# Kernel optimization log

Hardware: AMD Instinct MI355X
Metric: run time of the kernel (lower is better)

Reference implementation:

```python
import jax, jax.numpy as jnp
import numpy as np

EPS = 1e-5
NUM_HEADS = 8


def _ln(x, g, b):
    m = x.mean(-1, keepdims=True)
    v = jnp.mean((x - m) ** 2, -1, keepdims=True)
    return (x - m) * jax.lax.rsqrt(v + EPS) * g + b


def _bn(x, g, b, m, v):  # eval-mode BatchNorm2d on NCHW
    sh = (1, -1, 1, 1)
    return (x - m.reshape(sh)) * jax.lax.rsqrt(v.reshape(sh) + EPS) * g.reshape(sh) + b.reshape(sh)


def _conv3x3(x, w):
    return jax.lax.conv_general_dilated(x, w, (1, 1), 'SAME', dimension_numbers=('NCHW', 'OIHW', 'NCHW'))


def _gelu(x):
    return jax.nn.gelu(x, approximate=False)  # torch nn.GELU default (erf)


def _attention(x, w_qkv, temperature, w_proj):
    # XCiT-style cross-covariance (channel) attention
    B, N, C = x.shape
    h = NUM_HEADS
    d = C // h
    qkv = (x @ w_qkv.T).reshape(B, N, 3, h, d)
    qkv = jnp.transpose(qkv, (2, 0, 3, 4, 1))  # [3, B, h, d, N]
    q, k, v = qkv[0], qkv[1], qkv[2]
    q = q / jnp.maximum(jnp.linalg.norm(q, axis=-1, keepdims=True), 1e-12)
    k = k / jnp.maximum(jnp.linalg.norm(k, axis=-1, keepdims=True), 1e-12)
    attn = jnp.einsum('bhdn,bhen->bhde', q, k) * temperature[None, :, None, None]
    attn = jax.nn.softmax(attn, axis=-1)  # [B, h, d, d]
    out = jnp.einsum('bhde,bhen->bhdn', attn, v)
    out = jnp.transpose(out, (0, 3, 1, 2)).reshape(B, N, C)
    return out @ w_proj.T


def _forward(x, ln1_g, ln1_b, w_qkv, temperature, w_proj, gamma1,
             ln2_g, ln2_b, mlp_w1, bn1_g, bn1_b, bn1_m, bn1_v,
             mlp_w2, bn2_g, bn2_b, bn2_m, bn2_v, gamma2,
             ln3_g, ln3_b, pconv1, pbn_g, pbn_b, pbn_m, pbn_v, pconv2, gamma3,
             H, W):
    B, N, C = x.shape
    # --- Attention residual block ---
    z = _attention(_ln(x, ln1_g, ln1_b), w_qkv, temperature, w_proj)
    x = x + gamma1 * z
    # --- ConvMlp residual block (1x1 convs + eval BN) ---
    y = _ln(x, ln2_g, ln2_b)
    y = jnp.transpose(y, (0, 2, 1)).reshape(B, C, H, W)
    y = _bn(jnp.einsum('oc,bchw->bohw', mlp_w1, y), bn1_g, bn1_b, bn1_m, bn1_v)
    y = _gelu(y)
    y = _bn(jnp.einsum('oc,bchw->bohw', mlp_w2, y), bn2_g, bn2_b, bn2_m, bn2_v)
    y = jnp.transpose(y.reshape(B, C, N), (0, 2, 1))
    x = x + gamma2 * y
    # --- Projection residual block (3x3 conv + BN + GELU + 3x3 conv) ---
    p = _ln(x, ln3_g, ln3_b)
    p = jnp.transpose(p, (0, 2, 1)).reshape(B, C, H, W)
    p = _conv3x3(p, pconv1)
    p = _gelu(_bn(p, pbn_g, pbn_b, pbn_m, pbn_v))
    p = _conv3x3(p, pconv2)
    p = jnp.transpose(p.reshape(B, C, N), (0, 2, 1))
    x = x + gamma3 * p
    return x


def setup_inputs() -> dict:
    key = jax.random.key(0)
    B, H, W, C, MR = 16, 48, 48, 384, 2
    N = H * W
    C2 = C * MR
    ks = jax.random.split(key, 12)
    nrm = lambda k, sh, s: (jax.random.normal(k, sh) * s).astype(jnp.float32)
    INIT_VALUES = 1e-4  # ResidualBlock default gamma init
    return {
        'x': nrm(ks[0], (B, N, C), 1.0),
        'ln1_g': jnp.ones((C,), jnp.float32), 'ln1_b': jnp.zeros((C,), jnp.float32),
        'w_qkv': nrm(ks[1], (3 * C, C), C ** -0.5),
        'temperature': jnp.ones((NUM_HEADS,), jnp.float32),
        'w_proj': nrm(ks[2], (C, C), C ** -0.5),
        'gamma1': jnp.full((C,), INIT_VALUES, jnp.float32),
        'ln2_g': jnp.ones((C,), jnp.float32), 'ln2_b': jnp.zeros((C,), jnp.float32),
        'mlp_w1': nrm(ks[3], (C2, C), C ** -0.5),
        'bn1_g': jnp.ones((C2,), jnp.float32), 'bn1_b': jnp.zeros((C2,), jnp.float32),
        'bn1_m': nrm(ks[4], (C2,), 0.1), 'bn1_v': jnp.ones((C2,), jnp.float32),
        'mlp_w2': nrm(ks[5], (C, C2), C2 ** -0.5),
        'bn2_g': jnp.ones((C,), jnp.float32), 'bn2_b': jnp.zeros((C,), jnp.float32),
        'bn2_m': nrm(ks[6], (C,), 0.1), 'bn2_v': jnp.ones((C,), jnp.float32),
        'gamma2': jnp.full((C,), INIT_VALUES, jnp.float32),
        'ln3_g': jnp.ones((C,), jnp.float32), 'ln3_b': jnp.zeros((C,), jnp.float32),
        'pconv1': nrm(ks[7], (C, C, 3, 3), (9 * C) ** -0.5),
        'pbn_g': jnp.ones((C,), jnp.float32), 'pbn_b': jnp.zeros((C,), jnp.float32),
        'pbn_m': nrm(ks[8], (C,), 0.1), 'pbn_v': jnp.ones((C,), jnp.float32),
        'pconv2': nrm(ks[9], (C, C, 3, 3), (9 * C) ** -0.5),
        'gamma3': jnp.full((C,), INIT_VALUES, jnp.float32),
        'H': H, 'W': W,
    }


def reference(x, ln1_g, ln1_b, w_qkv, temperature, w_proj, gamma1,
              ln2_g, ln2_b, mlp_w1, bn1_g, bn1_b, bn1_m, bn1_v,
              mlp_w2, bn2_g, bn2_b, bn2_m, bn2_v, gamma2,
              ln3_g, ln3_b, pconv1, pbn_g, pbn_b, pbn_m, pbn_v, pconv2, gamma3,
              H, W):
    out = _forward(x, ln1_g, ln1_b, w_qkv, temperature, w_proj, gamma1,
                   ln2_g, ln2_b, mlp_w1, bn1_g, bn1_b, bn1_m, bn1_v,
                   mlp_w2, bn2_g, bn2_b, bn2_m, bn2_v, gamma2,
                   ln3_g, ln3_b, pconv1, pbn_g, pbn_b, pbn_m, pbn_v, pconv2, gamma3,
                   H, W)
    return (out, H, W)
```

## Files before the change

kernel.cpp:

```cpp
#include <hip/hip_runtime.h>
#include <hip/hip_bf16.h>

typedef unsigned short u16;
typedef unsigned char  u8;
typedef __attribute__((ext_vector_type(4))) float floatx4;

#define LN_EPS 1e-5f

__device__ __forceinline__ float bf2f(u16 u) {
    unsigned int i = ((unsigned int)u) << 16;
    float f; __builtin_memcpy(&f, &i, 4); return f;
}
__device__ __forceinline__ u16 f2bf(float f) {
    __hip_bfloat16 h = __float2bfloat16(f);
    u16 u; __builtin_memcpy(&u, &h, 2); return u;
}
__device__ __forceinline__ u8 f2e4(float f) {
    int p = __builtin_amdgcn_cvt_pk_fp8_f32(f, f, 0, false);
    return (u8)(p & 0xff);
}

__device__ __forceinline__ int swz(int m, int k) {
    return (k & ~63) | (((((k >> 3) + (m >> 1)) & 7) << 3)) | (k & 7);
}

__device__ __forceinline__ void gl_lds16(const u8* g, u8* l) {
    __builtin_amdgcn_global_load_lds(
        (const __attribute__((address_space(1))) void*)(const void*)g,
        (__attribute__((address_space(3))) void*)(void*)l,
        16, 0, 0);
}

__global__ void cvt_f2e4_kernel(const float* __restrict__ in, u8* __restrict__ out,
                                int n4, int Kp) {
    int i = blockIdx.x * blockDim.x + threadIdx.x;
    if (i < n4) {
        float4 f = ((const float4*)in)[i];
        uchar4 o; o.x = f2e4(f.x); o.y = f2e4(f.y); o.z = f2e4(f.z); o.w = f2e4(f.w);
        int e = i * 4;
        int n = e / Kp, k = e - n * Kp;
        *(uchar4*)(out + (size_t)n * Kp + swz(n, k)) = o;
    }
}

__global__ void zero_kernel(u16* __restrict__ p, int n) {
    int i = blockIdx.x * blockDim.x + threadIdx.x;
    if (i < n) p[i] = 0;
}

__global__ void zero_f32_kernel(float* __restrict__ p, int n) {
    int i = blockIdx.x * blockDim.x + threadIdx.x;
    if (i < n) p[i] = 0.f;
}

template<bool SWZ>
__global__ __launch_bounds__(64)
void ln_kernel(const float* __restrict__ xf, const float* __restrict__ g,
               const float* __restrict__ b, u8* __restrict__ out) {
    const int row = blockIdx.x;
    const int lane = threadIdx.x;
    const float* xr = xf + (size_t)row * 384;
    float v[6], s = 0.f, s2 = 0.f;
#pragma unroll
    for (int i = 0; i < 6; ++i) { v[i] = xr[lane + i * 64]; s += v[i]; s2 += v[i] * v[i]; }
#pragma unroll
    for (int off = 32; off; off >>= 1) { s += __shfl_xor(s, off); s2 += __shfl_xor(s2, off); }
    float mean = s * (1.0f / 384.0f);
    float var  = s2 * (1.0f / 384.0f) - mean * mean;
    float rstd = rsqrtf(var + LN_EPS);
    u8* orow = out + (size_t)row * 384;
    int pofs = lane;
    if (SWZ) {
        const int gperm = (row >> 1) & 7;
        pofs = ((((lane >> 3) + gperm) & 7) << 3) | (lane & 7);
    }
#pragma unroll
    for (int i = 0; i < 6; ++i) {
        int c = lane + i * 64;
        orow[i * 64 + pofs] = f2e4((v[i] - mean) * rstd * g[c] + b[c]);
    }
}

template<int ACONV, int EPI, bool SWZO = false>
__global__ __launch_bounds__(256, 4)
void gemm_nt(const u8* __restrict__ A, const u8* __restrict__ Bm,
             int M, int N, int K,
             u16* __restrict__ Obf, int ldo,
             float* __restrict__ xf, float* __restrict__ ofb, const float* __restrict__ xin,
             const float* __restrict__ bn_g, const float* __restrict__ bn_b,
             const float* __restrict__ bn_m, const float* __restrict__ bn_v,
             const float* __restrict__ gamma, const u8* __restrict__ zp) {
    __shared__ u8 As[2][128 * 64];
    __shared__ u8 Bs[2][128 * 64];

    const int tid = threadIdx.x;
    const int gx = gridDim.x;
    const int g  = blockIdx.y * gx + blockIdx.x;
    const int G  = gx * gridDim.y;
    int L = g;
    if ((G & 7) == 0) L = (g & 7) * (G >> 3) + (g >> 3);
    const int n0 = (L % gx) * 128;
    const int m0 = (L / gx) * 128;

    const int lane  = tid & 63;
    const int wave  = tid >> 6;
    const int wm    = (wave >> 1) * 64;
    const int wn    = (wave & 1) * 64;
    const int fr    = lane & 15;
    const int klane = lane >> 4;

    int arow[4], brow[4];
#pragma unroll
    for (int i = 0; i < 4; ++i) {
        arow[i] = (wm + i * 16 + fr) * 64;
        brow[i] = (wn + i * 16 + fr) * 64;
    }
    int csw8[2];
#pragma unroll
    for (int kh = 0; kh < 2; ++kh)
        csw8[kh] = ((((kh << 2) + klane) + (fr >> 1)) & 7) << 3;
    int csw4[2];
#pragma unroll
    for (int kh = 0; kh < 2; ++kh)
        csw4[kh] = ((((kh << 1) + (klane >> 1) + (fr >> 1)) & 3) << 4) + ((klane & 1) << 3);

    const int srow = tid >> 2;
    const int scol = (tid & 3) << 4;
    const int ssc4 = ((((tid & 3) - ((tid >> 3) & 3)) & 3) << 4);
    const u8 *sa[2], *sb[2];
    const u8* imgq[2];
    int ay[2], ax[2];
#pragma unroll
    for (int q = 0; q < 2; ++q) {
        int r = q * 64 + srow;
        if (ACONV == 0) {
            sa[q] = A + (size_t)(m0 + r) * K + scol;
        } else {
            int nA = m0 + r;
            int bi = nA / 2304;
            int nl = nA - bi * 2304;
            ay[q] = nl / 48;
            ax[q] = nl - ay[q] * 48;
            imgq[q] = A + (size_t)bi * 2304 * 384;
        }
        sb[q] = Bm + (size_t)(n0 + q * 64 + srow) * K + scol;
    }

    int scnt = 0, sjj = 0;
    const int NT = K / 64;

    auto STAGE = [&](int d) {
        if (ACONV == 1) {
            if (scnt == 0) {
                int t3 = sjj / 3;
                int dy = t3 - 1, dx = sjj - t3 * 3 - 1;
                ++sjj;
#pragma unroll
                for (int q = 0; q < 2; ++q) {
                    int yy = ay[q] + dy, xx = ax[q] + dx;
                    bool v = ((unsigned)yy < 48u) & ((unsigned)xx < 48u);
                    sa[q] = (v ? imgq[q] + (size_t)(yy * 48 + xx) * 384 : zp) + ssc4;
                }
            }
            scnt = (scnt == 5) ? 0 : scnt + 1;
        }
        u8* la = &As[d][0];
        u8* lb = &Bs[d][0];
        gl_lds16(sa[0], la + ((wave * 64) << 4));        sa[0] += 64;
        gl_lds16(sa[1], la + ((256 + wave * 64) << 4));  sa[1] += 64;
        gl_lds16(sb[0], lb + ((wave * 64) << 4));        sb[0] += 64;
        gl_lds16(sb[1], lb + ((256 + wave * 64) << 4));  sb[1] += 64;
    };

    floatx4 acc[4][4];
#pragma unroll
    for (int i = 0; i < 4; ++i)
#pragma unroll
        for (int j = 0; j < 4; ++j) acc[i][j] = (floatx4){0.f, 0.f, 0.f, 0.f};

    STAGE(0);
    STAGE(1);
    asm volatile("s_waitcnt vmcnt(4)" ::: "memory");
    __builtin_amdgcn_s_barrier();
    asm volatile("" ::: "memory");

    int cur = 0;
    for (int t = 0; t < NT; ++t) {
        const u8* Ab = &As[cur][0];
        const u8* Bb = &Bs[cur][0];
#pragma unroll
        for (int kh = 0; kh < 2; ++kh) {
            long af[4], bfr[4];
#pragma unroll
            for (int i = 0; i < 4; ++i) af[i]  = *(const long*)(Ab + arow[i] + (ACONV ? csw4[kh] : csw8[kh]));
#pragma unroll
            for (int j = 0; j < 4; ++j)  bfr[j] = *(const long*)(Bb + brow[j] + csw8[kh]);
#pragma unroll
            for (int i = 0; i < 4; ++i)
#pragma unroll
                for (int j = 0; j < 4; ++j)
                    acc[i][j] = __builtin_amdgcn_mfma_f32_16x16x32_fp8_fp8(af[i], bfr[j], acc[i][j], 0, 0, 0);
        }
        asm volatile("s_waitcnt lgkmcnt(0)" ::: "memory");
        __builtin_amdgcn_s_barrier();
        asm volatile("" ::: "memory");
        if (t + 2 < NT) {
            STAGE(cur);
            asm volatile("s_waitcnt vmcnt(4)" ::: "memory");
        } else {
            asm volatile("s_waitcnt vmcnt(0)" ::: "memory");
        }
        __builtin_amdgcn_sched_barrier(0);
        __builtin_amdgcn_s_barrier();
        asm volatile("" ::: "memory");
        cur ^= 1;
    }

    const int quad4 = (lane >> 4) * 4;
#pragma unroll
    for (int j = 0; j < 4; ++j) {
        int col = n0 + wn + j * 16 + fr;
        float bscale = 0.f, bshift = 0.f, gam = 0.f;
        if (EPI == 1 || EPI == 2) {
            bscale = bn_g[col] * rsqrtf(bn_v[col] + LN_EPS);
            bshift = bn_b[col] - bn_m[col] * bscale;
        }
        if (EPI >= 2) gam = gamma[col];
#pragma unroll
        for (int i = 0; i < 4; ++i) {
#pragma unroll
            for (int r = 0; r < 4; ++r) {
                int row = m0 + wm + i * 16 + quad4 + r;
                float v = acc[i][j][r];
                if (EPI == 0) {
                    Obf[(size_t)row * ldo + col] = f2bf(v);
                } else if (EPI == 1) {
                    float t = v * bscale + bshift;
                    t = 0.5f * t * (1.0f + erff(t * 0.70710678118654752f));
                    int oc = SWZO ? swz(row, col) : col;
                    ((u8*)Obf)[(size_t)row * ldo + oc] = f2e4(t);
                } else if (EPI == 2) {
                    float t = v * bscale + bshift;
                    xf[(size_t)row * N + col] += gam * t;
                } else if (EPI == 3) {
                    xf[(size_t)row * N + col] += gam * v;
                } else if (EPI == 4) {
                    ofb[(size_t)row * N + col] = xf[(size_t)row * N + col] + gam * v;
                } else {
                    xf[(size_t)row * N + col] = xin[(size_t)row * N + col] + gam * v;
                }
            }
        }
    }
}

__global__ __launch_bounds__(256)
void gram_kernel(const u16* __restrict__ qkv, float* __restrict__ Sacc,
                 float* __restrict__ nrm2) {
    const int bh = blockIdx.y;
    const int b = bh >> 3, h = bh & 7;
    const int tid = threadIdx.x;
    __shared__ float qsf[64][48];
    __shared__ float ksf[64][48];

    float acc9[3][3];
#pragma unroll
    for (int i = 0; i < 3; ++i)
#pragma unroll
        for (int j = 0; j < 3; ++j) acc9[i][j] = 0.f;
    float qn2 = 0.f, kn2 = 0.f;

    const int qoff = h * 48;
    const int koff = 384 + h * 48;
    const int d0 = (tid >> 4) * 3;
    const int e0 = (tid & 15) * 3;
    const int nbase = blockIdx.x * 128;

    for (int c = 0; c < 2; ++c) {
        const int n0 = nbase + c * 64;
#pragma unroll
        for (int it = 0; it < 6; ++it) {
            int chunk = tid + it * 256;
            int mat = chunk >= 768 ? 1 : 0;
            int rem = chunk - mat * 768;
            int nn = rem / 12, u = rem - nn * 12;
            ushort4 raw = *(const ushort4*)(qkv + (size_t)(b * 2304 + n0 + nn) * 1152 +
                                            (mat ? koff : qoff) + u * 4);
            float4 f = make_float4(bf2f(raw.x), bf2f(raw.y), bf2f(raw.z), bf2f(raw.w));
            if (mat) *(float4*)&ksf[nn][u * 4] = f;
            else     *(float4*)&qsf[nn][u * 4] = f;
        }
        __syncthreads();
#pragma unroll 4
        for (int nn = 0; nn < 64; ++nn) {
            float q0 = qsf[nn][d0], q1 = qsf[nn][d0 + 1], q2 = qsf[nn][d0 + 2];
            float k0v = ksf[nn][e0], k1v = ksf[nn][e0 + 1], k2v = ksf[nn][e0 + 2];
            acc9[0][0] += q0 * k0v; acc9[0][1] += q0 * k1v; acc9[0][2] += q0 * k2v;
            acc9[1][0] += q1 * k0v; acc9[1][1] += q1 * k1v; acc9[1][2] += q1 * k2v;
            acc9[2][0] += q2 * k0v; acc9[2][1] += q2 * k1v; acc9[2][2] += q2 * k2v;
        }
        if (tid < 48) {
            for (int nn = 0; nn < 64; ++nn) { float q = qsf[nn][tid]; qn2 += q * q; }
        } else if (tid >= 128 && tid < 176) {
            int e = tid - 128;
            for (int nn = 0; nn < 64; ++nn) { float k = ksf[nn][e]; kn2 += k * k; }
        }
        __syncthreads();
    }

    float* Sb = Sacc + (size_t)bh * 2304;
#pragma unroll
    for (int i = 0; i < 3; ++i)
#pragma unroll
        for (int j = 0; j < 3; ++j)
            atomicAdd(&Sb[(d0 + i) * 48 + e0 + j], acc9[i][j]);
    if (tid < 48) atomicAdd(&nrm2[bh * 96 + tid], qn2);
    else if (tid >= 128 && tid < 176) atomicAdd(&nrm2[bh * 96 + 48 + (tid - 128)], kn2);
}

__global__ __launch_bounds__(256)
void attn_fin_kernel(const float* __restrict__ Sacc, const float* __restrict__ nrm2,
                     const float* __restrict__ temp, float* __restrict__ attnb) {
    const int bh = blockIdx.x;
    const int h = bh & 7;
    const int tid = threadIdx.x;
    __shared__ float S[48][49];
    __shared__ float qns[48], kns[48];

    const float* Sb = Sacc + (size_t)bh * 2304;
    for (int i = tid; i < 2304; i += 256) {
        int d = i / 48, e = i - d * 48;
        S[d][e] = Sb[i];
    }
    if (tid < 48)      qns[tid]      = fmaxf(sqrtf(nrm2[bh * 96 + tid]), 1e-12f);
    else if (tid < 96) kns[tid - 48] = fmaxf(sqrtf(nrm2[bh * 96 + tid]), 1e-12f);
    __syncthreads();

    if (tid < 48) {
        float tf = temp[h] / qns[tid];
        float mx = -1e30f;
        for (int e = 0; e < 48; ++e) {
            float t = S[tid][e] * tf / kns[e];
            S[tid][e] = t;
            mx = fmaxf(mx, t);
        }
        float sum = 0.f;
        for (int e = 0; e < 48; ++e) { float t = __expf(S[tid][e] - mx); S[tid][e] = t; sum += t; }
        float inv = 1.0f / sum;
        float* dst = attnb + ((size_t)bh * 48 + tid) * 48;
        for (int e = 0; e < 48; ++e) dst[e] = S[tid][e] * inv;
    }
}

__global__ __launch_bounds__(256)
void attnout_kernel(const u16* __restrict__ qkv, const float* __restrict__ attnb,
                    u8* __restrict__ z) {
    const int r0 = blockIdx.x * 64;
    const int h  = blockIdx.y;
    const int b  = r0 / 2304;
    const int tid = threadIdx.x;
    __shared__ float A[48][49];
    __shared__ float vsf[64][48];

    const float* asrc = attnb + (size_t)(b * 8 + h) * 2304;
    for (int i = tid; i < 2304; i += 256) {
        int d = i / 48, e = i - d * 48;
        A[d][e] = asrc[i];
    }
    const int voff = 768 + h * 48;
    for (int i = tid; i < 768; i += 256) {
        int nn = i / 12, u = i - nn * 12;
        ushort4 raw = *(const ushort4*)(qkv + (size_t)(r0 + nn) * 1152 + voff + u * 4);
        float4 f = make_float4(bf2f(raw.x), bf2f(raw.y), bf2f(raw.z), bf2f(raw.w));
        *(float4*)&vsf[nn][u * 4] = f;
    }
    __syncthreads();

    const int rr0 = (tid >> 4) * 4;
    const int d0  = (tid & 15) * 3;
    float acc[4][3];
#pragma unroll
    for (int r = 0; r < 4; ++r)
#pragma unroll
        for (int j = 0; j < 3; ++j) acc[r][j] = 0.f;

#pragma unroll 4
    for (int e = 0; e < 48; ++e) {
        float a0 = A[d0][e], a1 = A[d0 + 1][e], a2 = A[d0 + 2][e];
#pragma unroll
        for (int r = 0; r < 4; ++r) {
            float vv = vsf[rr0 + r][e];
            acc[r][0] += a0 * vv; acc[r][1] += a1 * vv; acc[r][2] += a2 * vv;
        }
    }
#pragma unroll
    for (int r = 0; r < 4; ++r)
#pragma unroll
        for (int j = 0; j < 3; ++j) {
            int row = r0 + rr0 + r;
            int col = h * 48 + d0 + j;
            z[(size_t)row * 384 + swz(row, col)] = f2e4(acc[r][j]);
        }
}

__global__ void reorder_w_kernel(const float* __restrict__ w, u8* __restrict__ wr, int n) {
    int i = blockIdx.x * blockDim.x + threadIdx.x;
    if (i < n) {
        int o = i / 3456, rem = i - o * 3456;
        int j = rem / 384, c = rem - j * 384;
        wr[(size_t)o * 3456 + swz(o, rem)] = f2e4(w[(size_t)(o * 384 + c) * 9 + j]);
    }
}

__global__ void tail_kernel(const int* __restrict__ Hp, const int* __restrict__ Wp,
                            float* __restrict__ out, size_t base, int n_extra) {
    if (threadIdx.x == 0) {
        if (n_extra >= 1) out[base]     = (float)Hp[0];
        if (n_extra >= 2) out[base + 1] = (float)Wp[0];
    }
}

extern "C" void kernel_launch(void* const* d_in, const int* in_sizes, int n_in,
                              void* d_out, int out_size, void* d_ws, size_t ws_size,
                              hipStream_t stream) {
    const float* x      = (const float*)d_in[0];
    const float* ln1_g  = (const float*)d_in[1];
    const float* ln1_b  = (const float*)d_in[2];
    const float* w_qkv  = (const float*)d_in[3];
    const float* temp   = (const float*)d_in[4];
    const float* w_proj = (const float*)d_in[5];
    const float* gamma1 = (const float*)d_in[6];
    const float* ln2_g  = (const float*)d_in[7];
    const float* ln2_b  = (const float*)d_in[8];
    const float* mlp_w1 = (const float*)d_in[9];
    const float* bn1_g  = (const float*)d_in[10];
    const float* bn1_b  = (const float*)d_in[11];
    const float* bn1_m  = (const float*)d_in[12];
    const float* bn1_v  = (const float*)d_in[13];
    const float* mlp_w2 = (const float*)d_in[14];
    const float* bn2_g  = (const float*)d_in[15];
    const float* bn2_b  = (const float*)d_in[16];
    const float* bn2_m  = (const float*)d_in[17];
    const float* bn2_v  = (const float*)d_in[18];
    const float* gamma2 = (const float*)d_in[19];
    const float* ln3_g  = (const float*)d_in[20];
    const float* ln3_b  = (const float*)d_in[21];
    const float* pconv1 = (const float*)d_in[22];
    const float* pbn_g  = (const float*)d_in[23];
    const float* pbn_b  = (const float*)d_in[24];
    const float* pbn_m  = (const float*)d_in[25];
    const float* pbn_v  = (const float*)d_in[26];
    const float* pconv2 = (const float*)d_in[27];
    const float* gamma3 = (const float*)d_in[28];
    const int* Hp = (const int*)d_in[29];
    const int* Wp = (const int*)d_in[30];

    const int M = 36864, C = 384, C2 = 768, NQKV = 1152, KC = 3456;
    const size_t NBNC = (size_t)M * C;

    const size_t SZ_XF  = NBNC * 4;
    const size_t SZ_LN  = NBNC * 2;
    const size_t SZ_BIG = (size_t)M * NQKV * 2;
    const size_t SZ_P3  = SZ_LN;
    const size_t SZ_W   = (size_t)C * KC * 2;
    if (ws_size < SZ_XF + SZ_LN + SZ_BIG + SZ_P3 + 2 * SZ_W) return;

    char* ws = (char*)d_ws;
    float* xf     = (float*)ws;
    u8*    lnbuf  = (u8*)(ws + SZ_XF);
    u16*   big    = (u16*)(ws + SZ_XF + SZ_LN);
    char*  p3     = ws + SZ_XF + SZ_LN + SZ_BIG;
    float* attnb  = (float*)p3;
    u8*    wqkvb  = (u8*)(p3 + 1179648);
    u8*    wprojb = (u8*)(p3 + 1179648 + 884736);
    u8*    w1b    = (u8*)(p3 + 1179648 + 884736 + 294912);
    u8*    w2b    = (u8*)(p3 + 1179648 + 884736 + 294912 + 589824);
    float* Sacc   = (float*)(p3 + 3538944);
    float* nrm2   = (float*)(p3 + 3538944 + 1179648);
    u8*    convbf = (u8*)p3;
    u8*    w1r    = (u8*)(p3 + SZ_P3);
    u8*    w2r    = (u8*)(p3 + SZ_P3 + SZ_W);
    u8*    zp     = (u8*)big;

    const int n_extra = out_size - (int)NBNC;

    cvt_f2e4_kernel<<<(NQKV * C / 4 + 255) / 256, 256, 0, stream>>>(w_qkv, wqkvb, NQKV * C / 4, C);
    cvt_f2e4_kernel<<<(C * C / 4 + 255) / 256, 256, 0, stream>>>(w_proj, wprojb, C * C / 4, C);
    cvt_f2e4_kernel<<<(C2 * C / 4 + 255) / 256, 256, 0, stream>>>(mlp_w1, w1b, C2 * C / 4, C);
    cvt_f2e4_kernel<<<(C * C2 / 4 + 255) / 256, 256, 0, stream>>>(mlp_w2, w2b, C * C2 / 4, C2);
    zero_f32_kernel<<<(128 * 2304 + 128 * 96 + 255) / 256, 256, 0, stream>>>(
        Sacc, 128 * 2304 + 128 * 96);

    ln_kernel<true><<<M, 64, 0, stream>>>(x, ln1_g, ln1_b, lnbuf);
    gemm_nt<0, 0><<<dim3(NQKV / 128, M / 128), 256, 0, stream>>>(
        lnbuf, wqkvb, M, NQKV, C, big, NQKV, nullptr, nullptr, nullptr,
        nullptr, nullptr, nullptr, nullptr, nullptr, nullptr);
    gram_kernel<<<dim3(18, 128), 256, 0, stream>>>(big, Sacc, nrm2);
    attn_fin_kernel<<<128, 256, 0, stream>>>(Sacc, nrm2, temp, attnb);
    attnout_kernel<<<dim3(M / 64, 8), 256, 0, stream>>>(big, attnb, lnbuf);
    gemm_nt<0, 5><<<dim3(C / 128, M / 128), 256, 0, stream>>>(
        lnbuf, wprojb, M, C, C, nullptr, 0, xf, nullptr, x,
        nullptr, nullptr, nullptr, nullptr, gamma1, nullptr);

    ln_kernel<true><<<M, 64, 0, stream>>>(xf, ln2_g, ln2_b, lnbuf);
    gemm_nt<0, 1, true><<<dim3(C2 / 128, M / 128), 256, 0, stream>>>(
        lnbuf, w1b, M, C2, C, (u16*)big, C2, nullptr, nullptr, nullptr,
        bn1_g, bn1_b, bn1_m, bn1_v, nullptr, nullptr);
    gemm_nt<0, 2><<<dim3(C / 128, M / 128), 256, 0, stream>>>(
        (u8*)big, w2b, M, C, C2, nullptr, 0, xf, nullptr, nullptr,
        bn2_g, bn2_b, bn2_m, bn2_v, gamma2, nullptr);

    ln_kernel<false><<<M, 64, 0, stream>>>(xf, ln3_g, ln3_b, lnbuf);
    reorder_w_kernel<<<(C * KC + 255) / 256, 256, 0, stream>>>(pconv1, w1r, C * KC);
    reorder_w_kernel<<<(C * KC + 255) / 256, 256, 0, stream>>>(pconv2, w2r, C * KC);
    zero_kernel<<<8, 256, 0, stream>>>((u16*)zp, 2048);
    gemm_nt<1, 1, false><<<dim3(C / 128, M / 128), 256, 0, stream>>>(
        lnbuf, w1r, M, C, KC, (u16*)convbf, C, nullptr, nullptr, nullptr,
        pbn_g, pbn_b, pbn_m, pbn_v, nullptr, zp);
    gemm_nt<1, 4><<<dim3(C / 128, M / 128), 256, 0, stream>>>(
        convbf, w2r, M, C, KC, nullptr, 0, xf, (float*)d_out, nullptr,
        nullptr, nullptr, nullptr, nullptr, gamma3, zp);

    tail_kernel<<<1, 64, 0, stream>>>(Hp, Wp, (float*)d_out, NBNC, n_extra);
}
```

Measured before the change: 675.1 us.

## Fuse weight prep launches, batch LN rows per block, raise MFMA priority

Merges the weight conversions, conv weight reorder, zeroing and tail writes into one prep kernel launched up front, with the conv zero-pad moved into a dedicated workspace region. The LayerNorm kernel now handles four rows per 256-thread block instead of one row per 64-thread block. The GEMM main loop raises wave priority around the MFMA issue. The aim is less launch overhead and better scheduling, at the cost of a slightly larger workspace requirement.

```diff
diff --git a/kernel.cpp b/kernel.cpp
--- a/kernel.cpp
+++ b/kernel.cpp
@@ -31,34 +31,54 @@
         16, 0, 0);
 }
 
-__global__ void cvt_f2e4_kernel(const float* __restrict__ in, u8* __restrict__ out,
-                                int n4, int Kp) {
-    int i = blockIdx.x * blockDim.x + threadIdx.x;
-    if (i < n4) {
-        float4 f = ((const float4*)in)[i];
-        uchar4 o; o.x = f2e4(f.x); o.y = f2e4(f.y); o.z = f2e4(f.z); o.w = f2e4(f.w);
-        int e = i * 4;
-        int n = e / Kp, k = e - n * Kp;
-        *(uchar4*)(out + (size_t)n * Kp + swz(n, k)) = o;
-    }
-}
-
-__global__ void zero_kernel(u16* __restrict__ p, int n) {
-    int i = blockIdx.x * blockDim.x + threadIdx.x;
-    if (i < n) p[i] = 0;
-}
-
-__global__ void zero_f32_kernel(float* __restrict__ p, int n) {
-    int i = blockIdx.x * blockDim.x + threadIdx.x;
-    if (i < n) p[i] = 0.f;
-}
+__device__ __forceinline__ void cvt4_body(const float* __restrict__ in, u8* __restrict__ out,
+                                          int i, int Kp) {
+    float4 f = ((const float4*)in)[i];
+    uchar4 o; o.x = f2e4(f.x); o.y = f2e4(f.y); o.z = f2e4(f.z); o.w = f2e4(f.w);
+    int e = i * 4;
+    int n = e / Kp, k = e - n * Kp;
+    *(uchar4*)(out + (size_t)n * Kp + swz(n, k)) = o;
+}
+__device__ __forceinline__ void reord_body(const float* __restrict__ w, u8* __restrict__ wr,
+                                           int i) {
+    int o = i / 3456, rem = i - o * 3456;
+    int j = rem / 384, c = rem - j * 384;
+    wr[(size_t)o * 3456 + swz(o, rem)] = f2e4(w[(size_t)(o * 384 + c) * 9 + j]);
+}
+
+__global__ __launch_bounds__(256)
+void prep_kernel(const float* __restrict__ w_qkv, u8* __restrict__ wqkvb,
+                 const float* __restrict__ w_proj, u8* __restrict__ wprojb,
+                 const float* __restrict__ mlp_w1, u8* __restrict__ w1b,
+                 const float* __restrict__ mlp_w2, u8* __restrict__ w2b,
+                 float* __restrict__ Sacc,
+                 const float* __restrict__ pconv1, u8* __restrict__ w1r,
+                 const float* __restrict__ pconv2, u8* __restrict__ w2r,
+                 unsigned int* __restrict__ zp,
+                 const int* __restrict__ Hp, const int* __restrict__ Wp,
+                 float* __restrict__ dout, size_t base, int n_extra) {
+    int i = blockIdx.x * 256 + threadIdx.x;
+    if (i < 110592)                   { cvt4_body(w_qkv, wqkvb, i, 384);  return; }
+    if ((i -= 110592) < 36864)        { cvt4_body(w_proj, wprojb, i, 384); return; }
+    if ((i -= 36864) < 73728)         { cvt4_body(mlp_w1, w1b, i, 384);   return; }
+    if ((i -= 73728) < 73728)         { cvt4_body(mlp_w2, w2b, i, 768);   return; }
+    if ((i -= 73728) < 307200)        { Sacc[i] = 0.f;                    return; }
+    if ((i -= 307200) < 1327104)      { reord_body(pconv1, w1r, i);       return; }
+    if ((i -= 1327104) < 1327104)     { reord_body(pconv2, w2r, i);       return; }
+    if ((i -= 1327104) < 1024)        { zp[i] = 0u;                       return; }
+    if ((i -= 1024) < 2) {
+        if (i == 0 && n_extra >= 1) dout[base]     = (float)Hp[0];
+        if (i == 1 && n_extra >= 2) dout[base + 1] = (float)Wp[0];
+    }
+}
+#define PREP_TOTAL (110592 + 36864 + 73728 + 73728 + 307200 + 1327104 + 1327104 + 1024 + 2)
 
 template<bool SWZ>
-__global__ __launch_bounds__(64)
+__global__ __launch_bounds__(256)
 void ln_kernel(const float* __restrict__ xf, const float* __restrict__ g,
                const float* __restrict__ b, u8* __restrict__ out) {
-    const int row = blockIdx.x;
-    const int lane = threadIdx.x;
+    const int row = blockIdx.x * 4 + (threadIdx.x >> 6);
+    const int lane = threadIdx.x & 63;
     const float* xr = xf + (size_t)row * 384;
     float v[6], s = 0.f, s2 = 0.f;
 #pragma unroll
@@ -195,11 +215,13 @@
             for (int i = 0; i < 4; ++i) af[i]  = *(const long*)(Ab + arow[i] + (ACONV ? csw4[kh] : csw8[kh]));
 #pragma unroll
             for (int j = 0; j < 4; ++j)  bfr[j] = *(const long*)(Bb + brow[j] + csw8[kh]);
+            __builtin_amdgcn_s_setprio(1);
 #pragma unroll
             for (int i = 0; i < 4; ++i)
 #pragma unroll
                 for (int j = 0; j < 4; ++j)
                     acc[i][j] = __builtin_amdgcn_mfma_f32_16x16x32_fp8_fp8(af[i], bfr[j], acc[i][j], 0, 0, 0);
+            __builtin_amdgcn_s_setprio(0);
         }
         asm volatile("s_waitcnt lgkmcnt(0)" ::: "memory");
         __builtin_amdgcn_s_barrier();
@@ -401,23 +423,6 @@
             int col = h * 48 + d0 + j;
             z[(size_t)row * 384 + swz(row, col)] = f2e4(acc[r][j]);
         }
-}
-
-__global__ void reorder_w_kernel(const float* __restrict__ w, u8* __restrict__ wr, int n) {
-    int i = blockIdx.x * blockDim.x + threadIdx.x;
-    if (i < n) {
-        int o = i / 3456, rem = i - o * 3456;
-        int j = rem / 384, c = rem - j * 384;
-        wr[(size_t)o * 3456 + swz(o, rem)] = f2e4(w[(size_t)(o * 384 + c) * 9 + j]);
-    }
-}
-
-__global__ void tail_kernel(const int* __restrict__ Hp, const int* __restrict__ Wp,
-                            float* __restrict__ out, size_t base, int n_extra) {
-    if (threadIdx.x == 0) {
-        if (n_extra >= 1) out[base]     = (float)Hp[0];
-        if (n_extra >= 2) out[base + 1] = (float)Wp[0];
-    }
 }
 
 extern "C" void kernel_launch(void* const* d_in, const int* in_sizes, int n_in,
@@ -463,7 +468,7 @@
     const size_t SZ_BIG = (size_t)M * NQKV * 2;
     const size_t SZ_P3  = SZ_LN;
     const size_t SZ_W   = (size_t)C * KC * 2;
-    if (ws_size < SZ_XF + SZ_LN + SZ_BIG + SZ_P3 + 2 * SZ_W) return;
+    if (ws_size < SZ_XF + SZ_LN + SZ_BIG + SZ_P3 + 2 * SZ_W + 4096) return;
 
     char* ws = (char*)d_ws;
     float* xf     = (float*)ws;
@@ -480,18 +485,16 @@
     u8*    convbf = (u8*)p3;
     u8*    w1r    = (u8*)(p3 + SZ_P3);
     u8*    w2r    = (u8*)(p3 + SZ_P3 + SZ_W);
-    u8*    zp     = (u8*)big;
+    u8*    zpg    = (u8*)(p3 + SZ_P3 + 2 * SZ_W);
 
     const int n_extra = out_size - (int)NBNC;
 
-    cvt_f2e4_kernel<<<(NQKV * C / 4 + 255) / 256, 256, 0, stream>>>(w_qkv, wqkvb, NQKV * C / 4, C);
-    cvt_f2e4_kernel<<<(C * C / 4 + 255) / 256, 256, 0, stream>>>(w_proj, wprojb, C * C / 4, C);
-    cvt_f2e4_kernel<<<(C2 * C / 4 + 255) / 256, 256, 0, stream>>>(mlp_w1, w1b, C2 * C / 4, C);
-    cvt_f2e4_kernel<<<(C * C2 / 4 + 255) / 256, 256, 0, stream>>>(mlp_w2, w2b, C * C2 / 4, C2);
-    zero_f32_kernel<<<(128 * 2304 + 128 * 96 + 255) / 256, 256, 0, stream>>>(
-        Sacc, 128 * 2304 + 128 * 96);
-
-    ln_kernel<true><<<M, 64, 0, stream>>>(x, ln1_g, ln1_b, lnbuf);
+    prep_kernel<<<(PREP_TOTAL + 255) / 256, 256, 0, stream>>>(
+        w_qkv, wqkvb, w_proj, wprojb, mlp_w1, w1b, mlp_w2, w2b,
+        Sacc, pconv1, w1r, pconv2, w2r, (unsigned int*)zpg,
+        Hp, Wp, (float*)d_out, NBNC, n_extra);
+
+    ln_kernel<true><<<M / 4, 256, 0, stream>>>(x, ln1_g, ln1_b, lnbuf);
     gemm_nt<0, 0><<<dim3(NQKV / 128, M / 128), 256, 0, stream>>>(
         lnbuf, wqkvb, M, NQKV, C, big, NQKV, nullptr, nullptr, nullptr,
         nullptr, nullptr, nullptr, nullptr, nullptr, nullptr);
@@ -502,7 +505,7 @@
         lnbuf, wprojb, M, C, C, nullptr, 0, xf, nullptr, x,
         nullptr, nullptr, nullptr, nullptr, gamma1, nullptr);
 
-    ln_kernel<true><<<M, 64, 0, stream>>>(xf, ln2_g, ln2_b, lnbuf);
+    ln_kernel<true><<<M / 4, 256, 0, stream>>>(xf, ln2_g, ln2_b, lnbuf);
     gemm_nt<0, 1, true><<<dim3(C2 / 128, M / 128), 256, 0, stream>>>(
         lnbuf, w1b, M, C2, C, (u16*)big, C2, nullptr, nullptr, nullptr,
         bn1_g, bn1_b, bn1_m, bn1_v, nullptr, nullptr);
@@ -510,16 +513,11 @@
         (u8*)big, w2b, M, C, C2, nullptr, 0, xf, nullptr, nullptr,
         bn2_g, bn2_b, bn2_m, bn2_v, gamma2, nullptr);
 
-    ln_kernel<false><<<M, 64, 0, stream>>>(xf, ln3_g, ln3_b, lnbuf);
-    reorder_w_kernel<<<(C * KC + 255) / 256, 256, 0, stream>>>(pconv1, w1r, C * KC);
-    reorder_w_kernel<<<(C * KC + 255) / 256, 256, 0, stream>>>(pconv2, w2r, C * KC);
-    zero_kernel<<<8, 256, 0, stream>>>((u16*)zp, 2048);
+    ln_kernel<false><<<M / 4, 256, 0, stream>>>(xf, ln3_g, ln3_b, lnbuf);
     gemm_nt<1, 1, false><<<dim3(C / 128, M / 128), 256, 0, stream>>>(
         lnbuf, w1r, M, C, KC, (u16*)convbf, C, nullptr, nullptr, nullptr,
-        pbn_g, pbn_b, pbn_m, pbn_v, nullptr, zp);
+        pbn_g, pbn_b, pbn_m, pbn_v, nullptr, zpg);
     gemm_nt<1, 4><<<dim3(C / 128, M / 128), 256, 0, stream>>>(
         convbf, w2r, M, C, KC, nullptr, 0, xf, (float*)d_out, nullptr,
-        nullptr, nullptr, nullptr, nullptr, gamma3, zp);
-
-    tail_kernel<<<1, 64, 0, stream>>>(Hp, Wp, (float*)d_out, NBNC, n_extra);
-}
+        nullptr, nullptr, nullptr, nullptr, gamma3, zpg);
+}
```

Result: faster. 655.0 us (-3.0%).
